# Performance work log

Hardware: AMD Instinct MI355X
Metric: run time of the kernel (lower is better)

The kernel has to match this reference:

```python
import jax, jax.numpy as jnp
import numpy as np

B, S, D, H, L, F = 4, 2048, 512, 8, 4, 2048
DH = D // H
EPS = 1e-5


def setup_inputs() -> dict:
    key = jax.random.key(0)
    ks = jax.random.split(key, 16)
    sc = 0.02
    inp = {
        "turn_embeddings": jax.random.normal(ks[0], (B, S, D), jnp.float32),
        "Wqkv": jax.random.normal(ks[1], (L, 3 * D, D), jnp.float32) * sc,
        "bqkv": jnp.zeros((L, 3 * D), jnp.float32),
        "Wo": jax.random.normal(ks[2], (L, D, D), jnp.float32) * sc,
        "bo": jnp.zeros((L, D), jnp.float32),
        "W1": jax.random.normal(ks[3], (L, F, D), jnp.float32) * sc,
        "b1": jnp.zeros((L, F), jnp.float32),
        "W2": jax.random.normal(ks[4], (L, D, F), jnp.float32) * sc,
        "b2": jnp.zeros((L, D), jnp.float32),
        "ln1_g": jnp.ones((L, D), jnp.float32),
        "ln1_b": jnp.zeros((L, D), jnp.float32),
        "ln2_g": jnp.ones((L, D), jnp.float32),
        "ln2_b": jnp.zeros((L, D), jnp.float32),
        "speaker_ids": jax.random.randint(ks[5], (B, S), 0, 4, jnp.int64 if jax.config.jax_enable_x64 else jnp.int32),
    }
    return inp


def _layer_norm(x, g, b):
    mu = jnp.mean(x, axis=-1, keepdims=True)
    var = jnp.mean(jnp.square(x - mu), axis=-1, keepdims=True)
    return (x - mu) * jax.lax.rsqrt(var + EPS) * g + b


def _attention(x, Wqkv, bqkv, Wo, bo, allow):
    # x: [B,S,D]; allow: [B,1,S,S] boolean (causal & same-speaker)
    qkv = x @ Wqkv.T + bqkv                       # [B,S,3D]
    q, k, v = jnp.split(qkv, 3, axis=-1)
    q = q.reshape(x.shape[0], x.shape[1], H, DH)
    k = k.reshape(x.shape[0], x.shape[1], H, DH)
    v = v.reshape(x.shape[0], x.shape[1], H, DH)
    scores = jnp.einsum("bqhd,bkhd->bhqk", q, k) / np.sqrt(DH)
    scores = jnp.where(allow, scores, jnp.finfo(scores.dtype).min)
    p = jax.nn.softmax(scores, axis=-1)
    o = jnp.einsum("bhqk,bkhd->bqhd", p, v).reshape(x.shape[0], x.shape[1], D)
    return o @ Wo.T + bo


def reference(turn_embeddings, Wqkv, bqkv, Wo, bo, W1, b1, W2, b2,
              ln1_g, ln1_b, ln2_g, ln2_b, speaker_ids):
    Bc, Sc, _ = turn_embeddings.shape
    causal = jnp.tril(jnp.ones((Sc, Sc), bool))                 # [S,S]
    same = speaker_ids[:, :, None] == speaker_ids[:, None, :]    # [B,S,S]
    allow = (same & causal)[:, None, :, :]                       # [B,1,S,S]
    x = turn_embeddings
    for l in range(L):
        a = _attention(x, Wqkv[l], bqkv[l], Wo[l], bo[l], allow)
        x = _layer_norm(x + a, ln1_g[l], ln1_b[l])
        h = jax.nn.relu(x @ W1[l].T + b1[l]) @ W2[l].T + b2[l]
        x = _layer_norm(x + h, ln2_g[l], ln2_b[l])
    return x
```

## Files before the change

kernel.cpp:

```cpp
#include <hip/hip_runtime.h>
#include <stdint.h>

#define BN 4
#define SN 2048
#define DN 512
#define HN 8
#define LN 4
#define FN 2048
#define MN (BN * SN)
#define TD (3 * DN)

typedef __attribute__((ext_vector_type(8))) __bf16 bf16x8;
typedef __attribute__((ext_vector_type(4))) float f32x4;
typedef __attribute__((ext_vector_type(8))) unsigned short ushortx8;

static __device__ __forceinline__ unsigned short f2bf(float f) {
    return __builtin_bit_cast(unsigned short, (__bf16)f);
}
static __device__ __forceinline__ float bf2f(unsigned short h) {
    return __builtin_bit_cast(float, (uint32_t)h << 16);
}

static __device__ __forceinline__ void gload16(const void* g, void* l) {
    __builtin_amdgcn_global_load_lds(
        (const __attribute__((address_space(1))) void*)g,
        (__attribute__((address_space(3))) void*)l, 16, 0, 0);
}

__global__ __launch_bounds__(256) void k_cvt(const float* __restrict__ src,
                                             unsigned short* __restrict__ dst,
                                             int n4) {
    int i = blockIdx.x * blockDim.x + threadIdx.x;
    int stride = gridDim.x * blockDim.x;
    for (; i < n4; i += stride) {
        float4 v = ((const float4*)src)[i];
        ushort4 o;
        o.x = f2bf(v.x); o.y = f2bf(v.y); o.z = f2bf(v.z); o.w = f2bf(v.w);
        ((ushort4*)dst)[i] = o;
    }
}

template <int MODE>
__global__ __launch_bounds__(256) void k_gemm(const unsigned short* __restrict__ A,
                                              const unsigned short* __restrict__ B,
                                              const float* __restrict__ bias,
                                              float* __restrict__ Cf,
                                              unsigned short* __restrict__ Cb,
                                              int M, int N, int K, int GX) {
    __shared__ __align__(16) unsigned short As[128][64];
    __shared__ __align__(16) unsigned short Bs[128][64];

    const int t = threadIdx.x;
    const int lane = t & 63;
    const int wid = t >> 6;
    const int wm = wid >> 1, wn = wid & 1;
    const int lr = lane & 15;
    const int lg = lane >> 4;

    const int nwg = gridDim.x;
    const int bid = blockIdx.x;
    const int swz = (bid & 7) * (nwg >> 3) + (bid >> 3);
    const int bx = swz % GX;
    const int by = swz / GX;

    const size_t rowA = (size_t)by * 128;
    const size_t rowB = (size_t)bx * 128;
    const unsigned short* Ab = A + rowA * K;
    const unsigned short* Bb = B + rowB * K;

    const int srow = lane >> 3;
    const int sgran = (lane & 7) ^ srow;

    f32x4 acc[4][4] = {};

    for (int k0 = 0; k0 < K; k0 += 64) {
        __syncthreads();
#pragma unroll
        for (int j = 0; j < 4; ++j) {
            const int c = wid * 4 + j;
            const size_t goff = (size_t)(8 * c + srow) * K + k0 + sgran * 8;
            gload16(Ab + goff, &As[8 * c][0]);
            gload16(Bb + goff, &Bs[8 * c][0]);
        }
        __syncthreads();

#pragma unroll
        for (int h = 0; h < 2; ++h) {
            bf16x8 af[4], bfr[4];
#pragma unroll
            for (int mi = 0; mi < 4; ++mi) {
                const int gp = (h * 4 + lg) ^ (lr & 7);
                af[mi] = *(const bf16x8*)&As[wm * 64 + mi * 16 + lr][gp * 8];
            }
#pragma unroll
            for (int ni = 0; ni < 4; ++ni) {
                const int gp = (h * 4 + lg) ^ (lr & 7);
                bfr[ni] = *(const bf16x8*)&Bs[wn * 64 + ni * 16 + lr][gp * 8];
            }
#pragma unroll
            for (int mi = 0; mi < 4; ++mi)
#pragma unroll
                for (int ni = 0; ni < 4; ++ni)
                    acc[mi][ni] = __builtin_amdgcn_mfma_f32_16x16x32_bf16(
                        af[mi], bfr[ni], acc[mi][ni], 0, 0, 0);
        }
    }

    float bv[4];
#pragma unroll
    for (int ni = 0; ni < 4; ++ni)
        bv[ni] = bias[(int)rowB + wn * 64 + ni * 16 + lr];

#pragma unroll
    for (int mi = 0; mi < 4; ++mi) {
#pragma unroll
        for (int ni = 0; ni < 4; ++ni) {
            int col = (int)rowB + wn * 64 + ni * 16 + lr;
            int row0 = (int)rowA + wm * 64 + mi * 16 + ((lane >> 4) << 2);
#pragma unroll
            for (int r = 0; r < 4; ++r) {
                float v = acc[mi][ni][r] + bv[ni];
                if (MODE == 2) v = fmaxf(v, 0.f);
                if (MODE == 0)
                    Cf[(size_t)(row0 + r) * N + col] = v;
                else
                    Cb[(size_t)(row0 + r) * N + col] = f2bf(v);
            }
        }
    }
}

__global__ __launch_bounds__(256) void k_attn(const unsigned short* __restrict__ qkv,
                                              const int* __restrict__ spk,
                                              unsigned short* __restrict__ o) {
    __shared__ __align__(16) unsigned short Ks[2][64][72];
    __shared__ __align__(16) unsigned short Vt[2][64][72];
    __shared__ __align__(16) unsigned short Ps[4][16][72];

    const int t = threadIdx.x;
    const int lane = t & 63;
    const int w = t >> 6;
    const int lr = lane & 15;
    const int lg = lane >> 4;

    const int wg = blockIdx.x;
    const int inner = wg >> 3;
    const int bh = 4 * (wg & 7) + (inner & 3);
    const int qtile = (SN / 64 - 1) - (inner >> 2);
    const int b = bh >> 3;
    const int h = bh & 7;
    const int qb = qtile * 64;

    const size_t base = (size_t)b * SN * TD;
    const unsigned short* kg = qkv + base + DN + h * 64;
    const unsigned short* vg = qkv + base + 2 * DN + h * 64;

    const float SCL = 0.125f * 1.4426950408889634f;
    const unsigned short* qptr = qkv + base + (size_t)(qb + w * 16 + lr) * TD + h * 64;
    bf16x8 aq0 = *(const bf16x8*)(qptr + lg * 8);
    bf16x8 aq1 = *(const bf16x8*)(qptr + 32 + lg * 8);
#pragma unroll
    for (int j = 0; j < 8; ++j) {
        aq0[j] = (__bf16)((float)aq0[j] * SCL);
        aq1[j] = (__bf16)((float)aq1[j] * SCL);
    }

    int sqr[4], qrow[4];
#pragma unroll
    for (int r = 0; r < 4; ++r) {
        qrow[r] = qb + w * 16 + lg * 4 + r;
        sqr[r] = spk[b * SN + qrow[r]];
    }

    const int kr0 = t >> 3;
    const int kc0 = (t & 7) << 3;
    const int vrow = t & 63;
    const int vd0 = (t >> 6) * 16;

    uint4 kra = *(const uint4*)&kg[(size_t)kr0 * TD + kc0];
    uint4 krb = *(const uint4*)&kg[(size_t)(kr0 + 32) * TD + kc0];
    ushortx8 vra = *(const ushortx8*)&vg[(size_t)vrow * TD + vd0];
    ushortx8 vrb = *(const ushortx8*)&vg[(size_t)vrow * TD + vd0 + 8];
    *(uint4*)&Ks[0][kr0][kc0] = kra;
    *(uint4*)&Ks[0][kr0 + 32][kc0] = krb;
#pragma unroll
    for (int j = 0; j < 8; ++j) {
        Vt[0][vd0 + j][vrow] = vra[j];
        Vt[0][vd0 + 8 + j][vrow] = vrb[j];
    }

    float lsum[4] = {0.f, 0.f, 0.f, 0.f};
    f32x4 acc_o[4] = {};

    const int ntiles = qtile + 1;
    for (int it = 0; it < ntiles; ++it) {
        const int k0 = it * 64;
        const int cur = it & 1;
        __syncthreads();

        const bool nx = (it + 1 < ntiles);
        if (nx) {
            const int kn = k0 + 64;
            kra = *(const uint4*)&kg[(size_t)(kn + kr0) * TD + kc0];
            krb = *(const uint4*)&kg[(size_t)(kn + kr0 + 32) * TD + kc0];
            vra = *(const ushortx8*)&vg[(size_t)(kn + vrow) * TD + vd0];
            vrb = *(const ushortx8*)&vg[(size_t)(kn + vrow) * TD + vd0 + 8];
        }
        int skr[4];
#pragma unroll
        for (int ni = 0; ni < 4; ++ni) skr[ni] = spk[b * SN + k0 + 16 * ni + lr];

        f32x4 sc4[4] = {};
#pragma unroll
        for (int ni = 0; ni < 4; ++ni) {
            bf16x8 bk0 = *(const bf16x8*)&Ks[cur][16 * ni + lr][lg * 8];
            bf16x8 bk1 = *(const bf16x8*)&Ks[cur][16 * ni + lr][lg * 8 + 32];
            sc4[ni] = __builtin_amdgcn_mfma_f32_16x16x32_bf16(aq0, bk0, sc4[ni], 0, 0, 0);
            sc4[ni] = __builtin_amdgcn_mfma_f32_16x16x32_bf16(aq1, bk1, sc4[ni], 0, 0, 0);
        }

        const bool diag = (it == ntiles - 1);
#pragma unroll
        for (int ni = 0; ni < 4; ++ni) {
#pragma unroll
            for (int r = 0; r < 4; ++r) {
                bool allow = (skr[ni] == sqr[r]);
                if (diag) allow = allow && (16 * ni + lr <= w * 16 + lg * 4 + r);
                float p = allow ? exp2f(sc4[ni][r]) : 0.f;
                lsum[r] += p;
                Ps[w][lg * 4 + r][16 * ni + lr] = f2bf(p);
            }
        }

        bf16x8 ap0 = *(const bf16x8*)&Ps[w][lr][lg * 8];
        bf16x8 ap1 = *(const bf16x8*)&Ps[w][lr][lg * 8 + 32];
#pragma unroll
        for (int ni = 0; ni < 4; ++ni) {
            bf16x8 bv0 = *(const bf16x8*)&Vt[cur][16 * ni + lr][lg * 8];
            bf16x8 bv1 = *(const bf16x8*)&Vt[cur][16 * ni + lr][lg * 8 + 32];
            acc_o[ni] = __builtin_amdgcn_mfma_f32_16x16x32_bf16(ap0, bv0, acc_o[ni], 0, 0, 0);
            acc_o[ni] = __builtin_amdgcn_mfma_f32_16x16x32_bf16(ap1, bv1, acc_o[ni], 0, 0, 0);
        }

        if (nx) {
            const int nb = cur ^ 1;
            *(uint4*)&Ks[nb][kr0][kc0] = kra;
            *(uint4*)&Ks[nb][kr0 + 32][kc0] = krb;
#pragma unroll
            for (int j = 0; j < 8; ++j) {
                Vt[nb][vd0 + j][vrow] = vra[j];
                Vt[nb][vd0 + 8 + j][vrow] = vrb[j];
            }
        }
    }

#pragma unroll
    for (int r = 0; r < 4; ++r) {
        float s = lsum[r];
        s += __shfl_xor(s, 1);
        s += __shfl_xor(s, 2);
        s += __shfl_xor(s, 4);
        s += __shfl_xor(s, 8);
        float inv = 1.f / s;
#pragma unroll
        for (int ni = 0; ni < 4; ++ni) {
            int d = 16 * ni + lr;
            o[(size_t)(b * SN + qrow[r]) * DN + h * 64 + d] = f2bf(acc_o[ni][r] * inv);
        }
    }
}

__global__ __launch_bounds__(256) void k_add_ln(const float* xin, const float* dl,
                                                const float* __restrict__ g,
                                                const float* __restrict__ bta,
                                                float* xout,
                                                unsigned short* __restrict__ xb) {
    const int row = blockIdx.x * 4 + (threadIdx.x >> 6);
    const int lane = threadIdx.x & 63;
    const size_t off = (size_t)row * DN + lane * 8;
    const int c0 = lane * 8;

    float4 a0 = *(const float4*)&xin[off];
    float4 a1 = *(const float4*)&xin[off + 4];
    float4 d0 = *(const float4*)&dl[off];
    float4 d1 = *(const float4*)&dl[off + 4];
    float v[8] = {a0.x + d0.x, a0.y + d0.y, a0.z + d0.z, a0.w + d0.w,
                  a1.x + d1.x, a1.y + d1.y, a1.z + d1.z, a1.w + d1.w};
    float s1 = 0.f, s2 = 0.f;
#pragma unroll
    for (int i = 0; i < 8; ++i) { s1 += v[i]; s2 += v[i] * v[i]; }
#pragma unroll
    for (int msk = 32; msk; msk >>= 1) {
        s1 += __shfl_xor(s1, msk);
        s2 += __shfl_xor(s2, msk);
    }
    const float mean = s1 * (1.f / 512.f);
    const float var = s2 * (1.f / 512.f) - mean * mean;
    const float rs = rsqrtf(var + 1e-5f);

    float4 g0 = *(const float4*)&g[c0];
    float4 g1 = *(const float4*)&g[c0 + 4];
    float4 b0 = *(const float4*)&bta[c0];
    float4 b1 = *(const float4*)&bta[c0 + 4];
    float gg[8] = {g0.x, g0.y, g0.z, g0.w, g1.x, g1.y, g1.z, g1.w};
    float bb[8] = {b0.x, b0.y, b0.z, b0.w, b1.x, b1.y, b1.z, b1.w};

    float y[8];
    ushortx8 ub;
#pragma unroll
    for (int i = 0; i < 8; ++i) {
        y[i] = (v[i] - mean) * rs * gg[i] + bb[i];
        ub[i] = f2bf(y[i]);
    }
    *(float4*)&xout[off] = make_float4(y[0], y[1], y[2], y[3]);
    *(float4*)&xout[off + 4] = make_float4(y[4], y[5], y[6], y[7]);
    *(ushortx8*)&xb[off] = ub;
}

extern "C" void kernel_launch(void* const* d_in, const int* in_sizes, int n_in,
                              void* d_out, int out_size, void* d_ws, size_t ws_size,
                              hipStream_t stream) {
    const float* te   = (const float*)d_in[0];
    const float* Wqkv = (const float*)d_in[1];
    const float* bqkv = (const float*)d_in[2];
    const float* Wo   = (const float*)d_in[3];
    const float* bo   = (const float*)d_in[4];
    const float* W1   = (const float*)d_in[5];
    const float* b1   = (const float*)d_in[6];
    const float* W2   = (const float*)d_in[7];
    const float* b2   = (const float*)d_in[8];
    const float* g1   = (const float*)d_in[9];
    const float* be1  = (const float*)d_in[10];
    const float* g2   = (const float*)d_in[11];
    const float* be2  = (const float*)d_in[12];
    const int*   spk  = (const int*)d_in[13];
    float* out = (float*)d_out;

    char* ws = (char*)d_ws;
    size_t off = 0;
    auto alloc = [&](size_t bytes) -> char* {
        char* p = ws + off;
        off += (bytes + 255) & ~(size_t)255;
        return p;
    };
    unsigned short* wqkv_b = (unsigned short*)alloc((size_t)LN * TD * DN * 2);
    unsigned short* wo_b   = (unsigned short*)alloc((size_t)LN * DN * DN * 2);
    unsigned short* w1_b   = (unsigned short*)alloc((size_t)LN * FN * DN * 2);
    unsigned short* w2_b   = (unsigned short*)alloc((size_t)LN * DN * FN * 2);
    float*          x      = (float*)alloc((size_t)MN * DN * 4);
    unsigned short* xb     = (unsigned short*)alloc((size_t)MN * DN * 2);
    unsigned short* u      = (unsigned short*)alloc((size_t)MN * FN * 2);
    unsigned short* ob     = (unsigned short*)alloc((size_t)MN * DN * 2);
    float*          proj   = (float*)alloc((size_t)MN * DN * 4);
    unsigned short* qkvb = u;
    unsigned short* hb   = u;

    k_cvt<<<2048, 256, 0, stream>>>(Wqkv, wqkv_b, LN * TD * DN / 4);
    k_cvt<<<2048, 256, 0, stream>>>(Wo,   wo_b,   LN * DN * DN / 4);
    k_cvt<<<2048, 256, 0, stream>>>(W1,   w1_b,   LN * FN * DN / 4);
    k_cvt<<<2048, 256, 0, stream>>>(W2,   w2_b,   LN * DN * FN / 4);
    k_cvt<<<2048, 256, 0, stream>>>(te,   xb,     MN * DN / 4);

    for (int l = 0; l < LN; ++l) {
        k_gemm<1><<<(TD / 128) * (MN / 128), 256, 0, stream>>>(
            xb, wqkv_b + (size_t)l * TD * DN, bqkv + l * TD, nullptr, qkvb,
            MN, TD, DN, TD / 128);
        k_attn<<<(SN / 64) * BN * HN, 256, 0, stream>>>(qkvb, spk, ob);
        k_gemm<0><<<(DN / 128) * (MN / 128), 256, 0, stream>>>(
            ob, wo_b + (size_t)l * DN * DN, bo + l * DN, proj, nullptr,
            MN, DN, DN, DN / 128);
        k_add_ln<<<MN / 4, 256, 0, stream>>>(
            l == 0 ? te : x, proj, g1 + l * DN, be1 + l * DN, x, xb);
        k_gemm<2><<<(FN / 128) * (MN / 128), 256, 0, stream>>>(
            xb, w1_b + (size_t)l * FN * DN, b1 + l * FN, nullptr, hb,
            MN, FN, DN, FN / 128);
        k_gemm<0><<<(DN / 128) * (MN / 128), 256, 0, stream>>>(
            hb, w2_b + (size_t)l * DN * FN, b2 + l * DN, proj, nullptr,
            MN, DN, FN, DN / 128);
        k_add_ln<<<MN / 4, 256, 0, stream>>>(
            x, proj, g2 + l * DN, be2 + l * DN, (l == LN - 1) ? out : x, xb);
    }
    (void)in_sizes; (void)n_in; (void)out_size; (void)ws_size;
}
```

Baseline: 692.9 us.

## Widen attention query tile, narrow N=512 GEMM tiles, keep residual stream in bf16

Attention now gives each block 128 query rows, two 16-row groups per wave, so every K/V tile loaded into LDS is reused for twice as many queries. Tiles that lie entirely above a wave's causal diagonal are skipped, and s_setprio is raised around the MFMA sections. The output-projection and FFN2 GEMMs use 64-wide N tiles to launch more blocks, and they write bf16 instead of fp32. The fp32 residual buffer is dropped: the residual is carried in bf16 and fp32 is written only for the final output, which lowers precision in exchange for less memory traffic.

Result: slower. 848.4 us (+22.4%).

```diff
diff --git a/kernel.cpp b/kernel.cpp
--- a/kernel.cpp
+++ b/kernel.cpp
@@ -40,15 +40,15 @@
     }
 }
 
-template <int MODE>
+template <int MODE, int BNT>
 __global__ __launch_bounds__(256) void k_gemm(const unsigned short* __restrict__ A,
                                               const unsigned short* __restrict__ B,
                                               const float* __restrict__ bias,
-                                              float* __restrict__ Cf,
                                               unsigned short* __restrict__ Cb,
                                               int M, int N, int K, int GX) {
     __shared__ __align__(16) unsigned short As[128][64];
-    __shared__ __align__(16) unsigned short Bs[128][64];
+    __shared__ __align__(16) unsigned short Bs[BNT][64];
+    constexpr int NFR = BNT / 32;
 
     const int t = threadIdx.x;
     const int lane = t & 63;
@@ -64,14 +64,14 @@
     const int by = swz / GX;
 
     const size_t rowA = (size_t)by * 128;
-    const size_t rowB = (size_t)bx * 128;
+    const size_t rowB = (size_t)bx * BNT;
     const unsigned short* Ab = A + rowA * K;
     const unsigned short* Bb = B + rowB * K;
 
     const int srow = lane >> 3;
     const int sgran = (lane & 7) ^ srow;
 
-    f32x4 acc[4][4] = {};
+    f32x4 acc[4][NFR] = {};
 
     for (int k0 = 0; k0 < K; k0 += 64) {
         __syncthreads();
@@ -80,51 +80,50 @@
             const int c = wid * 4 + j;
             const size_t goff = (size_t)(8 * c + srow) * K + k0 + sgran * 8;
             gload16(Ab + goff, &As[8 * c][0]);
+        }
+#pragma unroll
+        for (int j = 0; j < NFR; ++j) {
+            const int c = wid * NFR + j;
+            const size_t goff = (size_t)(8 * c + srow) * K + k0 + sgran * 8;
             gload16(Bb + goff, &Bs[8 * c][0]);
         }
         __syncthreads();
 
 #pragma unroll
         for (int h = 0; h < 2; ++h) {
-            bf16x8 af[4], bfr[4];
-#pragma unroll
-            for (int mi = 0; mi < 4; ++mi) {
-                const int gp = (h * 4 + lg) ^ (lr & 7);
+            const int gp = (h * 4 + lg) ^ (lr & 7);
+            bf16x8 af[4], bfr[NFR];
+#pragma unroll
+            for (int mi = 0; mi < 4; ++mi)
                 af[mi] = *(const bf16x8*)&As[wm * 64 + mi * 16 + lr][gp * 8];
-            }
-#pragma unroll
-            for (int ni = 0; ni < 4; ++ni) {
-                const int gp = (h * 4 + lg) ^ (lr & 7);
-                bfr[ni] = *(const bf16x8*)&Bs[wn * 64 + ni * 16 + lr][gp * 8];
-            }
+#pragma unroll
+            for (int ni = 0; ni < NFR; ++ni)
+                bfr[ni] = *(const bf16x8*)&Bs[wn * (BNT / 2) + ni * 16 + lr][gp * 8];
 #pragma unroll
             for (int mi = 0; mi < 4; ++mi)
 #pragma unroll
-                for (int ni = 0; ni < 4; ++ni)
+                for (int ni = 0; ni < NFR; ++ni)
                     acc[mi][ni] = __builtin_amdgcn_mfma_f32_16x16x32_bf16(
                         af[mi], bfr[ni], acc[mi][ni], 0, 0, 0);
         }
     }
 
-    float bv[4];
-#pragma unroll
-    for (int ni = 0; ni < 4; ++ni)
-        bv[ni] = bias[(int)rowB + wn * 64 + ni * 16 + lr];
+    float bv[NFR];
+#pragma unroll
+    for (int ni = 0; ni < NFR; ++ni)
+        bv[ni] = bias[(int)rowB + wn * (BNT / 2) + ni * 16 + lr];
 
 #pragma unroll
     for (int mi = 0; mi < 4; ++mi) {
 #pragma unroll
-        for (int ni = 0; ni < 4; ++ni) {
-            int col = (int)rowB + wn * 64 + ni * 16 + lr;
-            int row0 = (int)rowA + wm * 64 + mi * 16 + ((lane >> 4) << 2);
+        for (int ni = 0; ni < NFR; ++ni) {
+            int col = (int)rowB + wn * (BNT / 2) + ni * 16 + lr;
+            int row0 = (int)rowA + wm * 64 + mi * 16 + lg * 4;
 #pragma unroll
             for (int r = 0; r < 4; ++r) {
                 float v = acc[mi][ni][r] + bv[ni];
                 if (MODE == 2) v = fmaxf(v, 0.f);
-                if (MODE == 0)
-                    Cf[(size_t)(row0 + r) * N + col] = v;
-                else
-                    Cb[(size_t)(row0 + r) * N + col] = f2bf(v);
+                Cb[(size_t)(row0 + r) * N + col] = f2bf(v);
             }
         }
     }
@@ -135,7 +134,7 @@
                                               unsigned short* __restrict__ o) {
     __shared__ __align__(16) unsigned short Ks[2][64][72];
     __shared__ __align__(16) unsigned short Vt[2][64][72];
-    __shared__ __align__(16) unsigned short Ps[4][16][72];
+    __shared__ __align__(16) unsigned short Ps[4][32][72];
 
     const int t = threadIdx.x;
     const int lane = t & 63;
@@ -146,31 +145,38 @@
     const int wg = blockIdx.x;
     const int inner = wg >> 3;
     const int bh = 4 * (wg & 7) + (inner & 3);
-    const int qtile = (SN / 64 - 1) - (inner >> 2);
+    const int qsuper = (SN / 128 - 1) - (inner >> 2);
     const int b = bh >> 3;
     const int h = bh & 7;
-    const int qb = qtile * 64;
+    const int qb = qsuper * 128;
 
     const size_t base = (size_t)b * SN * TD;
     const unsigned short* kg = qkv + base + DN + h * 64;
     const unsigned short* vg = qkv + base + 2 * DN + h * 64;
 
     const float SCL = 0.125f * 1.4426950408889634f;
-    const unsigned short* qptr = qkv + base + (size_t)(qb + w * 16 + lr) * TD + h * 64;
-    bf16x8 aq0 = *(const bf16x8*)(qptr + lg * 8);
-    bf16x8 aq1 = *(const bf16x8*)(qptr + 32 + lg * 8);
-#pragma unroll
-    for (int j = 0; j < 8; ++j) {
-        aq0[j] = (__bf16)((float)aq0[j] * SCL);
-        aq1[j] = (__bf16)((float)aq1[j] * SCL);
-    }
-
-    int sqr[4], qrow[4];
-#pragma unroll
-    for (int r = 0; r < 4; ++r) {
-        qrow[r] = qb + w * 16 + lg * 4 + r;
-        sqr[r] = spk[b * SN + qrow[r]];
-    }
+    bf16x8 aq[2][2];
+#pragma unroll
+    for (int g = 0; g < 2; ++g) {
+        const unsigned short* qptr =
+            qkv + base + (size_t)(qb + w * 32 + g * 16 + lr) * TD + h * 64;
+        aq[g][0] = *(const bf16x8*)(qptr + lg * 8);
+        aq[g][1] = *(const bf16x8*)(qptr + 32 + lg * 8);
+#pragma unroll
+        for (int j = 0; j < 8; ++j) {
+            aq[g][0][j] = (__bf16)((float)aq[g][0][j] * SCL);
+            aq[g][1][j] = (__bf16)((float)aq[g][1][j] * SCL);
+        }
+    }
+
+    int sqr[2][4], qrow[2][4];
+#pragma unroll
+    for (int g = 0; g < 2; ++g)
+#pragma unroll
+        for (int r = 0; r < 4; ++r) {
+            qrow[g][r] = qb + w * 32 + g * 16 + lg * 4 + r;
+            sqr[g][r] = spk[b * SN + qrow[g][r]];
+        }
 
     const int kr0 = t >> 3;
     const int kc0 = (t & 7) << 3;
@@ -189,10 +195,11 @@
         Vt[0][vd0 + 8 + j][vrow] = vrb[j];
     }
 
-    float lsum[4] = {0.f, 0.f, 0.f, 0.f};
-    f32x4 acc_o[4] = {};
-
-    const int ntiles = qtile + 1;
+    float lsum[2][4] = {};
+    f32x4 acc_o[2][4] = {};
+
+    const int ntiles = qb / 64 + 2;
+    const int qmax_w = qb + w * 32 + 31;
     for (int it = 0; it < ntiles; ++it) {
         const int k0 = it * 64;
         const int cur = it & 1;
@@ -206,40 +213,64 @@
             vra = *(const ushortx8*)&vg[(size_t)(kn + vrow) * TD + vd0];
             vrb = *(const ushortx8*)&vg[(size_t)(kn + vrow) * TD + vd0 + 8];
         }
-        int skr[4];
-#pragma unroll
-        for (int ni = 0; ni < 4; ++ni) skr[ni] = spk[b * SN + k0 + 16 * ni + lr];
-
-        f32x4 sc4[4] = {};
-#pragma unroll
-        for (int ni = 0; ni < 4; ++ni) {
-            bf16x8 bk0 = *(const bf16x8*)&Ks[cur][16 * ni + lr][lg * 8];
-            bf16x8 bk1 = *(const bf16x8*)&Ks[cur][16 * ni + lr][lg * 8 + 32];
-            sc4[ni] = __builtin_amdgcn_mfma_f32_16x16x32_bf16(aq0, bk0, sc4[ni], 0, 0, 0);
-            sc4[ni] = __builtin_amdgcn_mfma_f32_16x16x32_bf16(aq1, bk1, sc4[ni], 0, 0, 0);
-        }
-
-        const bool diag = (it == ntiles - 1);
-#pragma unroll
-        for (int ni = 0; ni < 4; ++ni) {
-#pragma unroll
-            for (int r = 0; r < 4; ++r) {
-                bool allow = (skr[ni] == sqr[r]);
-                if (diag) allow = allow && (16 * ni + lr <= w * 16 + lg * 4 + r);
-                float p = allow ? exp2f(sc4[ni][r]) : 0.f;
-                lsum[r] += p;
-                Ps[w][lg * 4 + r][16 * ni + lr] = f2bf(p);
-            }
-        }
-
-        bf16x8 ap0 = *(const bf16x8*)&Ps[w][lr][lg * 8];
-        bf16x8 ap1 = *(const bf16x8*)&Ps[w][lr][lg * 8 + 32];
-#pragma unroll
-        for (int ni = 0; ni < 4; ++ni) {
-            bf16x8 bv0 = *(const bf16x8*)&Vt[cur][16 * ni + lr][lg * 8];
-            bf16x8 bv1 = *(const bf16x8*)&Vt[cur][16 * ni + lr][lg * 8 + 32];
-            acc_o[ni] = __builtin_amdgcn_mfma_f32_16x16x32_bf16(ap0, bv0, acc_o[ni], 0, 0, 0);
-            acc_o[ni] = __builtin_amdgcn_mfma_f32_16x16x32_bf16(ap1, bv1, acc_o[ni], 0, 0, 0);
+
+        if (k0 <= qmax_w) {
+            int skr[4];
+#pragma unroll
+            for (int ni = 0; ni < 4; ++ni) skr[ni] = spk[b * SN + k0 + 16 * ni + lr];
+
+            f32x4 sc4[2][4] = {};
+            __builtin_amdgcn_s_setprio(1);
+#pragma unroll
+            for (int ni = 0; ni < 4; ++ni) {
+                bf16x8 bk0 = *(const bf16x8*)&Ks[cur][16 * ni + lr][lg * 8];
+                bf16x8 bk1 = *(const bf16x8*)&Ks[cur][16 * ni + lr][lg * 8 + 32];
+#pragma unroll
+                for (int g = 0; g < 2; ++g) {
+                    sc4[g][ni] = __builtin_amdgcn_mfma_f32_16x16x32_bf16(
+                        aq[g][0], bk0, sc4[g][ni], 0, 0, 0);
+                    sc4[g][ni] = __builtin_amdgcn_mfma_f32_16x16x32_bf16(
+                        aq[g][1], bk1, sc4[g][ni], 0, 0, 0);
+                }
+            }
+            __builtin_amdgcn_s_setprio(0);
+
+            const bool needC = (k0 + 63 >= qb + w * 32);
+#pragma unroll
+            for (int g = 0; g < 2; ++g) {
+#pragma unroll
+                for (int ni = 0; ni < 4; ++ni) {
+#pragma unroll
+                    for (int r = 0; r < 4; ++r) {
+                        bool allow = (skr[ni] == sqr[g][r]);
+                        if (needC) allow = allow && (k0 + 16 * ni + lr <= qrow[g][r]);
+                        float p = allow ? exp2f(sc4[g][ni][r]) : 0.f;
+                        lsum[g][r] += p;
+                        Ps[w][g * 16 + lg * 4 + r][16 * ni + lr] = f2bf(p);
+                    }
+                }
+            }
+
+            bf16x8 ap[2][2];
+#pragma unroll
+            for (int g = 0; g < 2; ++g) {
+                ap[g][0] = *(const bf16x8*)&Ps[w][g * 16 + lr][lg * 8];
+                ap[g][1] = *(const bf16x8*)&Ps[w][g * 16 + lr][lg * 8 + 32];
+            }
+            __builtin_amdgcn_s_setprio(1);
+#pragma unroll
+            for (int ni = 0; ni < 4; ++ni) {
+                bf16x8 bv0 = *(const bf16x8*)&Vt[cur][16 * ni + lr][lg * 8];
+                bf16x8 bv1 = *(const bf16x8*)&Vt[cur][16 * ni + lr][lg * 8 + 32];
+#pragma unroll
+                for (int g = 0; g < 2; ++g) {
+                    acc_o[g][ni] = __builtin_amdgcn_mfma_f32_16x16x32_bf16(
+                        ap[g][0], bv0, acc_o[g][ni], 0, 0, 0);
+                    acc_o[g][ni] = __builtin_amdgcn_mfma_f32_16x16x32_bf16(
+                        ap[g][1], bv1, acc_o[g][ni], 0, 0, 0);
+                }
+            }
+            __builtin_amdgcn_s_setprio(0);
         }
 
         if (nx) {
@@ -255,37 +286,52 @@
     }
 
 #pragma unroll
-    for (int r = 0; r < 4; ++r) {
-        float s = lsum[r];
-        s += __shfl_xor(s, 1);
-        s += __shfl_xor(s, 2);
-        s += __shfl_xor(s, 4);
-        s += __shfl_xor(s, 8);
-        float inv = 1.f / s;
-#pragma unroll
-        for (int ni = 0; ni < 4; ++ni) {
-            int d = 16 * ni + lr;
-            o[(size_t)(b * SN + qrow[r]) * DN + h * 64 + d] = f2bf(acc_o[ni][r] * inv);
-        }
-    }
-}
-
-__global__ __launch_bounds__(256) void k_add_ln(const float* xin, const float* dl,
+    for (int g = 0; g < 2; ++g)
+#pragma unroll
+        for (int r = 0; r < 4; ++r) {
+            float s = lsum[g][r];
+            s += __shfl_xor(s, 1);
+            s += __shfl_xor(s, 2);
+            s += __shfl_xor(s, 4);
+            s += __shfl_xor(s, 8);
+            float inv = 1.f / s;
+#pragma unroll
+            for (int ni = 0; ni < 4; ++ni) {
+                int d = 16 * ni + lr;
+                o[(size_t)(b * SN + qrow[g][r]) * DN + h * 64 + d] =
+                    f2bf(acc_o[g][ni][r] * inv);
+            }
+        }
+}
+
+template <bool XF32>
+__global__ __launch_bounds__(256) void k_add_ln(const void* __restrict__ xin_,
+                                                const unsigned short* __restrict__ dl,
                                                 const float* __restrict__ g,
                                                 const float* __restrict__ bta,
-                                                float* xout,
-                                                unsigned short* __restrict__ xb) {
+                                                unsigned short* __restrict__ xb,
+                                                float* __restrict__ fout) {
     const int row = blockIdx.x * 4 + (threadIdx.x >> 6);
     const int lane = threadIdx.x & 63;
     const size_t off = (size_t)row * DN + lane * 8;
     const int c0 = lane * 8;
 
-    float4 a0 = *(const float4*)&xin[off];
-    float4 a1 = *(const float4*)&xin[off + 4];
-    float4 d0 = *(const float4*)&dl[off];
-    float4 d1 = *(const float4*)&dl[off + 4];
-    float v[8] = {a0.x + d0.x, a0.y + d0.y, a0.z + d0.z, a0.w + d0.w,
-                  a1.x + d1.x, a1.y + d1.y, a1.z + d1.z, a1.w + d1.w};
+    float v[8];
+    if (XF32) {
+        const float* xin = (const float*)xin_;
+        float4 a0 = *(const float4*)&xin[off];
+        float4 a1 = *(const float4*)&xin[off + 4];
+        v[0] = a0.x; v[1] = a0.y; v[2] = a0.z; v[3] = a0.w;
+        v[4] = a1.x; v[5] = a1.y; v[6] = a1.z; v[7] = a1.w;
+    } else {
+        ushortx8 xa = *(const ushortx8*)&((const unsigned short*)xin_)[off];
+#pragma unroll
+        for (int i = 0; i < 8; ++i) v[i] = bf2f(xa[i]);
+    }
+    ushortx8 dd = *(const ushortx8*)&dl[off];
+#pragma unroll
+    for (int i = 0; i < 8; ++i) v[i] += bf2f(dd[i]);
+
     float s1 = 0.f, s2 = 0.f;
 #pragma unroll
     for (int i = 0; i < 8; ++i) { s1 += v[i]; s2 += v[i] * v[i]; }
@@ -312,9 +358,11 @@
         y[i] = (v[i] - mean) * rs * gg[i] + bb[i];
         ub[i] = f2bf(y[i]);
     }
-    *(float4*)&xout[off] = make_float4(y[0], y[1], y[2], y[3]);
-    *(float4*)&xout[off + 4] = make_float4(y[4], y[5], y[6], y[7]);
     *(ushortx8*)&xb[off] = ub;
+    if (fout) {
+        *(float4*)&fout[off] = make_float4(y[0], y[1], y[2], y[3]);
+        *(float4*)&fout[off + 4] = make_float4(y[4], y[5], y[6], y[7]);
+    }
 }
 
 extern "C" void kernel_launch(void* const* d_in, const int* in_sizes, int n_in,
@@ -347,11 +395,10 @@
     unsigned short* wo_b   = (unsigned short*)alloc((size_t)LN * DN * DN * 2);
     unsigned short* w1_b   = (unsigned short*)alloc((size_t)LN * FN * DN * 2);
     unsigned short* w2_b   = (unsigned short*)alloc((size_t)LN * DN * FN * 2);
-    float*          x      = (float*)alloc((size_t)MN * DN * 4);
     unsigned short* xb     = (unsigned short*)alloc((size_t)MN * DN * 2);
     unsigned short* u      = (unsigned short*)alloc((size_t)MN * FN * 2);
     unsigned short* ob     = (unsigned short*)alloc((size_t)MN * DN * 2);
-    float*          proj   = (float*)alloc((size_t)MN * DN * 4);
+    unsigned short* projb  = (unsigned short*)alloc((size_t)MN * DN * 2);
     unsigned short* qkvb = u;
     unsigned short* hb   = u;
 
@@ -362,23 +409,28 @@
     k_cvt<<<2048, 256, 0, stream>>>(te,   xb,     MN * DN / 4);
 
     for (int l = 0; l < LN; ++l) {
-        k_gemm<1><<<(TD / 128) * (MN / 128), 256, 0, stream>>>(
-            xb, wqkv_b + (size_t)l * TD * DN, bqkv + l * TD, nullptr, qkvb,
+        k_gemm<1, 128><<<(MN / 128) * (TD / 128), 256, 0, stream>>>(
+            xb, wqkv_b + (size_t)l * TD * DN, bqkv + l * TD, qkvb,
             MN, TD, DN, TD / 128);
-        k_attn<<<(SN / 64) * BN * HN, 256, 0, stream>>>(qkvb, spk, ob);
-        k_gemm<0><<<(DN / 128) * (MN / 128), 256, 0, stream>>>(
-            ob, wo_b + (size_t)l * DN * DN, bo + l * DN, proj, nullptr,
-            MN, DN, DN, DN / 128);
-        k_add_ln<<<MN / 4, 256, 0, stream>>>(
-            l == 0 ? te : x, proj, g1 + l * DN, be1 + l * DN, x, xb);
-        k_gemm<2><<<(FN / 128) * (MN / 128), 256, 0, stream>>>(
-            xb, w1_b + (size_t)l * FN * DN, b1 + l * FN, nullptr, hb,
+        k_attn<<<(SN / 128) * BN * HN, 256, 0, stream>>>(qkvb, spk, ob);
+        k_gemm<1, 64><<<(MN / 128) * (DN / 64), 256, 0, stream>>>(
+            ob, wo_b + (size_t)l * DN * DN, bo + l * DN, projb,
+            MN, DN, DN, DN / 64);
+        if (l == 0)
+            k_add_ln<true><<<MN / 4, 256, 0, stream>>>(
+                te, projb, g1 + l * DN, be1 + l * DN, xb, nullptr);
+        else
+            k_add_ln<false><<<MN / 4, 256, 0, stream>>>(
+                xb, projb, g1 + l * DN, be1 + l * DN, xb, nullptr);
+        k_gemm<2, 128><<<(MN / 128) * (FN / 128), 256, 0, stream>>>(
+            xb, w1_b + (size_t)l * FN * DN, b1 + l * FN, hb,
             MN, FN, DN, FN / 128);
-        k_gemm<0><<<(DN / 128) * (MN / 128), 256, 0, stream>>>(
-            hb, w2_b + (size_t)l * DN * FN, b2 + l * DN, proj, nullptr,
-            MN, DN, FN, DN / 128);
-        k_add_ln<<<MN / 4, 256, 0, stream>>>(
-            x, proj, g2 + l * DN, be2 + l * DN, (l == LN - 1) ? out : x, xb);
+        k_gemm<1, 64><<<(MN / 128) * (DN / 64), 256, 0, stream>>>(
+            hb, w2_b + (size_t)l * DN * FN, b2 + l * DN, projb,
+            MN, DN, FN, DN / 64);
+        k_add_ln<false><<<MN / 4, 256, 0, stream>>>(
+            xb, projb, g2 + l * DN, be2 + l * DN, xb,
+            (l == LN - 1) ? out : nullptr);
     }
     (void)in_sizes; (void)n_in; (void)out_size; (void)ws_size;
 }
```
